# Performance work log

Measured on AMD Instinct MI355X. Metric: run time of the kernel, lower is better.

The kernel has to match this reference:

```python
import jax, jax.numpy as jnp
import numpy as np

H, C, PQ, PV = 12, 16, 4, 8   # heads, c_hidden, qk points, v points
CS, CZ = 384, 128
INF, EPS = 1e5, 1e-8


def quat_to_rot(q):
    w, x, y, z = q[..., 0], q[..., 1], q[..., 2], q[..., 3]
    r = jnp.stack([
        1 - 2 * (y * y + z * z), 2 * (x * y - w * z), 2 * (x * z + w * y),
        2 * (x * y + w * z), 1 - 2 * (x * x + z * z), 2 * (y * z - w * x),
        2 * (x * z - w * y), 2 * (y * z + w * x), 1 - 2 * (x * x + y * y)],
        axis=-1)
    return r.reshape(q.shape[:-1] + (3, 3))


def setup_inputs() -> dict:
    key = jax.random.key(0)
    ks = jax.random.split(key, 20)
    B, N = 1, 768
    s = jax.random.normal(ks[0], (B, N, CS), jnp.float32)
    z = jax.random.normal(ks[1], (B, N, N, CZ), jnp.float32)
    quat = jax.random.normal(ks[2], (B, N, 4), jnp.float32)
    quat = quat / jnp.linalg.norm(quat, axis=-1, keepdims=True)
    rot = quat_to_rot(quat)
    trans = 10.0 * jax.random.normal(ks[3], (B, N, 3), jnp.float32)
    mask = jnp.ones((B, N), jnp.float32)
    ss = jax.random.uniform(ks[4], (B, N, N), jnp.float32)
    sc = 0.02
    W_q = sc * jax.random.normal(ks[5], (CS, H * C), jnp.float32)
    b_q = jnp.zeros((H * C,), jnp.float32)
    W_kv = sc * jax.random.normal(ks[6], (CS, 2 * H * C), jnp.float32)
    b_kv = jnp.zeros((2 * H * C,), jnp.float32)
    W_qp = sc * jax.random.normal(ks[7], (CS, H * PQ * 3), jnp.float32)
    b_qp = jnp.zeros((H * PQ * 3,), jnp.float32)
    W_kvp = sc * jax.random.normal(ks[8], (CS, H * (PQ + PV) * 3), jnp.float32)
    b_kvp = jnp.zeros((H * (PQ + PV) * 3,), jnp.float32)
    W_b = sc * jax.random.normal(ks[9], (CZ, H), jnp.float32)
    b_b = jnp.zeros((H,), jnp.float32)
    head_weights = 0.1 * jax.random.normal(ks[10], (H,), jnp.float32)
    cdim = H * (CZ + C + PV * 4)
    W_out = sc * jax.random.normal(ks[11], (cdim, CS), jnp.float32)
    b_out = jnp.zeros((CS,), jnp.float32)
    return dict(s=s, z=z, rot=rot, trans=trans, mask=mask, ss=ss,
                W_q=W_q, b_q=b_q, W_kv=W_kv, b_kv=b_kv, W_qp=W_qp, b_qp=b_qp,
                W_kvp=W_kvp, b_kvp=b_kvp, W_b=W_b, b_b=b_b,
                head_weights=head_weights, W_out=W_out, b_out=b_out)


def reference(s, z, rot, trans, mask, ss, W_q, b_q, W_kv, b_kv, W_qp, b_qp,
              W_kvp, b_kvp, W_b, b_b, head_weights, W_out, b_out):
    B, N, _ = s.shape
    # scalar q/k/v  [B,N,H,C]
    q = (s @ W_q + b_q).reshape(B, N, H, C)
    kv = (s @ W_kv + b_kv).reshape(B, N, H, 2 * C)
    k, v = kv[..., :C], kv[..., C:]
    # point q/k/v: linear output is [x_all, y_all, z_all] -> stack on last dim
    qp = s @ W_qp + b_qp                                  # [B,N,H*PQ*3]
    qp = jnp.stack(jnp.split(qp, 3, axis=-1), axis=-1)    # [B,N,H*PQ,3] local
    qp = jnp.einsum('bnxy,bnpy->bnpx', rot, qp) + trans[:, :, None]
    qp = qp.reshape(B, N, H, PQ, 3)                       # global frame
    kvp = s @ W_kvp + b_kvp
    kvp = jnp.stack(jnp.split(kvp, 3, axis=-1), axis=-1)  # [B,N,H*(PQ+PV),3]
    kvp = jnp.einsum('bnxy,bnpy->bnpx', rot, kvp) + trans[:, :, None]
    kvp = kvp.reshape(B, N, H, PQ + PV, 3)
    kp, vp = kvp[..., :PQ, :], kvp[..., PQ:, :]
    # scalar attention logits + pair bias
    b = z @ W_b + b_b                                     # [B,N,N,H]
    a = jnp.einsum('bihc,bjhc->bhij', q, k) * np.sqrt(1.0 / (3 * C))
    a = a + np.sqrt(1.0 / 3) * jnp.transpose(b, (0, 3, 1, 2))
    # point-distance attention
    diff = qp[:, :, None] - kp[:, None]                   # [B,N,N,H,PQ,3]
    d2 = jnp.sum(diff * diff, axis=-1)                    # [B,N,N,H,PQ]
    hw = jax.nn.softplus(head_weights) * np.sqrt(1.0 / (3 * (PQ * 9.0 / 2)))
    pt = -0.5 * jnp.sum(d2 * hw[None, None, None, :, None], axis=-1)  # [B,N,N,H]
    a = a + jnp.transpose(pt, (0, 3, 1, 2))
    sq_mask = INF * (mask[:, :, None] * mask[:, None, :] - 1.0)
    a = a + sq_mask[:, None]
    # weighted softmax (ss_usage='multiply', t_ss=1): weights = exp(ss) - 0.99
    weights = jnp.exp(ss) - 0.99                          # [B,N,N]
    e = jnp.exp(a - jnp.max(a, axis=-1, keepdims=True))
    we = e * weights[:, None]
    a = we / jnp.sum(we, axis=-1, keepdims=True)          # [B,H,N,N]
    # outputs
    o = jnp.einsum('bhij,bjhc->bihc', a, v).reshape(B, N, H * C)
    o_pt = jnp.einsum('bhij,bjhpc->bihpc', a, vp)         # [B,N,H,PV,3] global
    o_pt = jnp.einsum('bnyx,bnhpy->bnhpx', rot, o_pt - trans[:, :, None, None])
    o_pt_norm = jnp.sqrt(jnp.sum(o_pt ** 2, axis=-1) + EPS).reshape(B, N, H * PV)
    o_pt = o_pt.reshape(B, N, H * PV, 3)
    o_pair = jnp.einsum('bhij,bijc->bihc', a, z).reshape(B, N, H * CZ)
    cat = jnp.concatenate(
        [o, o_pt[..., 0], o_pt[..., 1], o_pt[..., 2], o_pt_norm, o_pair], axis=-1)
    return cat @ W_out + b_out
```

## Files before the change

kernel.cpp:

```cpp
#include <hip/hip_runtime.h>
#include <math.h>

#define NN 768
#define CSD 384
#define HD 12
#define CD 16
#define PQD 4
#define PVD 8
#define CZD 128
#define CATD 2112

#define OFF_Q      0u
#define OFF_K      147456u
#define OFF_V      294912u
#define OFF_QP     442368u
#define OFF_KP     552960u
#define OFF_VP     663552u
#define OFF_RAW    884736u
#define OFF_B      1327104u
#define OFF_A      8404992u
#define OFF_CAT    15482880u

__device__ __forceinline__ float wcol_val(const float* Wq, const float* Wkv,
                                          const float* Wqp, const float* Wkvp,
                                          int k, int col) {
  if (col < 192) return Wq[k*192 + col];
  if (col < 576) return Wkv[k*384 + (col-192)];
  if (col < 720) return Wqp[k*144 + (col-576)];
  return Wkvp[k*432 + (col-720)];
}
__device__ __forceinline__ float bias_val(const float* bq, const float* bkv,
                                          const float* bqp, const float* bkvp, int col) {
  if (col < 192) return bq[col];
  if (col < 576) return bkv[col-192];
  if (col < 720) return bqp[col-576];
  return bkvp[col-720];
}

__global__ __launch_bounds__(256) void k_proj(const float* __restrict__ s,
    const float* __restrict__ Wq, const float* __restrict__ bq,
    const float* __restrict__ Wkv, const float* __restrict__ bkv,
    const float* __restrict__ Wqp, const float* __restrict__ bqp,
    const float* __restrict__ Wkvp, const float* __restrict__ bkvp,
    float* __restrict__ ws) {
  __shared__ float At[64*17];
  __shared__ float Bt[16*64];
  int t = threadIdx.x;
  int c0 = blockIdx.x * 64;
  int r0 = blockIdx.y * 64;
  float acc[4][4] = {};
  int cc = t & 15, rr = t >> 4;
  for (int kt = 0; kt < CSD; kt += 16) {
    int ka = t & 15, mb = t >> 4;
#pragma unroll
    for (int p = 0; p < 4; ++p) {
      int m = mb + p*16;
      At[m*17 + ka] = s[(r0+m)*CSD + kt + ka];
    }
    int cb = t & 63, kb = t >> 6;
#pragma unroll
    for (int p = 0; p < 4; ++p) {
      int kk = kb + p*4;
      Bt[kk*64 + cb] = wcol_val(Wq,Wkv,Wqp,Wkvp, kt+kk, c0+cb);
    }
    __syncthreads();
#pragma unroll
    for (int k = 0; k < 16; ++k) {
      float a0 = At[(rr*4+0)*17 + k];
      float a1 = At[(rr*4+1)*17 + k];
      float a2 = At[(rr*4+2)*17 + k];
      float a3 = At[(rr*4+3)*17 + k];
      float4 b4 = *(const float4*)&Bt[k*64 + cc*4];
      acc[0][0] = fmaf(a0,b4.x,acc[0][0]); acc[0][1] = fmaf(a0,b4.y,acc[0][1]);
      acc[0][2] = fmaf(a0,b4.z,acc[0][2]); acc[0][3] = fmaf(a0,b4.w,acc[0][3]);
      acc[1][0] = fmaf(a1,b4.x,acc[1][0]); acc[1][1] = fmaf(a1,b4.y,acc[1][1]);
      acc[1][2] = fmaf(a1,b4.z,acc[1][2]); acc[1][3] = fmaf(a1,b4.w,acc[1][3]);
      acc[2][0] = fmaf(a2,b4.x,acc[2][0]); acc[2][1] = fmaf(a2,b4.y,acc[2][1]);
      acc[2][2] = fmaf(a2,b4.z,acc[2][2]); acc[2][3] = fmaf(a2,b4.w,acc[2][3]);
      acc[3][0] = fmaf(a3,b4.x,acc[3][0]); acc[3][1] = fmaf(a3,b4.y,acc[3][1]);
      acc[3][2] = fmaf(a3,b4.z,acc[3][2]); acc[3][3] = fmaf(a3,b4.w,acc[3][3]);
    }
    __syncthreads();
  }
  float* qbuf = ws + OFF_Q; float* kbuf = ws + OFF_K; float* vbuf = ws + OFF_V;
  float* raw  = ws + OFF_RAW;
#pragma unroll
  for (int jj = 0; jj < 4; ++jj) {
    int col = c0 + cc*4 + jj;
    float bv = bias_val(bq,bkv,bqp,bkvp,col);
#pragma unroll
    for (int ii = 0; ii < 4; ++ii) {
      int row = r0 + rr*4 + ii;
      float val = acc[ii][jj] + bv;
      if (col < 192) {
        int h = col >> 4, c = col & 15;
        qbuf[(h*NN + row)*CD + c] = val;
      } else if (col < 576) {
        int u = col - 192; int h = u >> 5; int c2 = u & 31;
        if (c2 < 16) kbuf[(h*NN+row)*CD + c2] = val;
        else         vbuf[(h*NN+row)*CD + (c2-16)] = val;
      } else {
        raw[row*576 + (col-576)] = val;
      }
    }
  }
}

__global__ __launch_bounds__(256) void k_points(const float* __restrict__ rot,
    const float* __restrict__ trans, const float* __restrict__ bout,
    float* __restrict__ out, float* __restrict__ ws) {
  int bx = blockIdx.x;
  if (bx >= 576) {
    int idx = (bx - 576)*256 + threadIdx.x;
    out[idx] = bout[idx % CSD];
    return;
  }
  int tg = bx*256 + threadIdx.x;
  int n = tg / 192, pidx = tg % 192;
  const float* raw = ws + OFF_RAW + n*576;
  float v0, v1, v2;
  if (pidx < 48) { v0 = raw[pidx]; v1 = raw[48+pidx]; v2 = raw[96+pidx]; }
  else { int pp = pidx-48; v0 = raw[144+pp]; v1 = raw[288+pp]; v2 = raw[432+pp]; }
  const float* R = rot + n*9; const float* T = trans + n*3;
  float g0 = R[0]*v0 + R[1]*v1 + R[2]*v2 + T[0];
  float g1 = R[3]*v0 + R[4]*v1 + R[5]*v2 + T[1];
  float g2 = R[6]*v0 + R[7]*v1 + R[8]*v2 + T[2];
  if (pidx < 48) {
    int h = pidx >> 2, p = pidx & 3;
    float* qp = ws + OFF_QP + ((h*NN + n)*PQD + p)*3;
    qp[0]=g0; qp[1]=g1; qp[2]=g2;
  } else {
    int pp = pidx - 48; int h = pp/12; int q12 = pp - 12*h;
    if (q12 < 4) { float* kp = ws + OFF_KP + ((h*NN+n)*PQD + q12)*3; kp[0]=g0; kp[1]=g1; kp[2]=g2; }
    else         { float* vp = ws + OFF_VP + ((h*NN+n)*PVD + (q12-4))*3; vp[0]=g0; vp[1]=g1; vp[2]=g2; }
  }
}

#define BR 128
#define BPAD 130
__global__ __launch_bounds__(256) void k_bias(const float* __restrict__ z,
    const float* __restrict__ Wb, const float* __restrict__ bb, float* __restrict__ ws) {
  __shared__ float zt[BR*BPAD];
  int t = threadIdx.x;
  int q = t & 15;
  int rg = t >> 4;
  float wbr[8][12];
#pragma unroll
  for (int cc = 0; cc < 8; ++cc) {
    const float* wp = Wb + (q*8 + cc)*HD;
#pragma unroll
    for (int h = 0; h < 12; ++h) wbr[cc][h] = wp[h];
  }
  const int b3=(q>>3)&1, b2=(q>>2)&1, b1=(q>>1)&1, b0=q&1;
  const int hmine = 6*b3 + 3*b2 + (b1 ? 2 : b0);
  const bool writer = !(b1 && b0);
  const float bbh = bb[hmine];

  const int rowbase = blockIdx.x * 1152;
  float* bmat = ws + OFF_B;
  const float s2 = 0.57735026918962576f;

  for (int T = 0; T < 9; ++T) {
    int r0 = rowbase + T*BR;
#pragma unroll 4
    for (int it = 0; it < 16; ++it) {
      int g = it*256 + t;
      int row = g >> 5, f4 = g & 31;
      float4 v = *(const float4*)(z + (size_t)(r0+row)*CZD + f4*4);
      float* d = &zt[row*BPAD + f4*4];
      *(float2*)(d)   = make_float2(v.x, v.y);
      *(float2*)(d+2) = make_float2(v.z, v.w);
    }
    __syncthreads();
#pragma unroll 2
    for (int ps = 0; ps < 8; ++ps) {
      int row = ps*16 + rg;
      const float* zr = &zt[row*BPAD + q*8];
      float2 z01 = *(const float2*)(zr);
      float2 z23 = *(const float2*)(zr+2);
      float2 z45 = *(const float2*)(zr+4);
      float2 z67 = *(const float2*)(zr+6);
      float acc[12];
#pragma unroll
      for (int h = 0; h < 12; ++h) {
        float a = z01.x*wbr[0][h];
        a = fmaf(z01.y, wbr[1][h], a);
        a = fmaf(z23.x, wbr[2][h], a);
        a = fmaf(z23.y, wbr[3][h], a);
        a = fmaf(z45.x, wbr[4][h], a);
        a = fmaf(z45.y, wbr[5][h], a);
        a = fmaf(z67.x, wbr[6][h], a);
        a = fmaf(z67.y, wbr[7][h], a);
        acc[h] = a;
      }
      float na[6];
#pragma unroll
      for (int m = 0; m < 6; ++m) {
        float keep = b3 ? acc[m+6] : acc[m];
        float give = b3 ? acc[m]   : acc[m+6];
        na[m] = keep + __shfl_xor(give, 8);
      }
      float nb[3];
#pragma unroll
      for (int m = 0; m < 3; ++m) {
        float keep = b2 ? na[m+3] : na[m];
        float give = b2 ? na[m]   : na[m+3];
        nb[m] = keep + __shfl_xor(give, 4);
      }
      float k0 = b1 ? nb[2] : nb[0];
      float g0v = b1 ? nb[0] : nb[2];
      float k1 = b1 ? 0.f   : nb[1];
      float g1v = b1 ? nb[1] : 0.f;
      float c0v = k0 + __shfl_xor(g0v, 2);
      float c1v = k1 + __shfl_xor(g1v, 2);
      float k2 = b1 ? c0v : (b0 ? c1v : c0v);
      float g2v = b1 ? c0v : (b0 ? c0v : c1v);
      float d0 = k2 + __shfl_xor(g2v, 1);
      if (writer) {
        int r = r0 + row;
        int i = r / NN;
        int j = r - i*NN;
        bmat[((size_t)i*HD + hmine)*NN + j] = s2*(d0 + bbh);
      }
    }
    __syncthreads();
  }
}

__global__ __launch_bounds__(256) void k_fused(
    const float* __restrict__ z,
    const float* __restrict__ rot, const float* __restrict__ trans,
    const float* __restrict__ mask, const float* __restrict__ ss,
    const float* __restrict__ hwts, float* __restrict__ ws) {
  __shared__ float a_sm[HD*NN];
  __shared__ float4 psm[2][HD][32];
  __shared__ float wred[8];
  int i = blockIdx.x;
  int t = threadIdx.x;
  const float* qbuf = ws + OFF_Q; const float* kbuf = ws + OFF_K;
  const float* qp   = ws + OFF_QP; const float* kp  = ws + OFF_KP;
  const float* vbuf = ws + OFF_V;  const float* vpbuf = ws + OFF_VP;
  const float* bmat = ws + OFF_B;
  float* cat = ws + OFF_CAT;
  const float s1 = 0.14433756729740643f;

  float mi = mask[i];
  float msk3[3], ss3[3];
#pragma unroll
  for (int jj = 0; jj < 3; ++jj) {
    int j = t + jj*256;
    msk3[jj] = 100000.0f*(mi*mask[j] - 1.0f);
    ss3[jj]  = __expf(ss[i*NN + j]) - 0.99f;
  }

  for (int h = 0; h < HD; ++h) {
    const float4* qv4 = (const float4*)(qbuf + (h*NN+i)*CD);
    float4 q0 = qv4[0], q1 = qv4[1], q2 = qv4[2], q3 = qv4[3];
    const float4* qp4 = (const float4*)(qp + (h*NN+i)*12);
    float4 p0 = qp4[0], p1 = qp4[1], p2 = qp4[2];
    float coef = -0.5f * 0.13608276348795434f * log1pf(__expf(hwts[h]));
    float l3[3];
#pragma unroll
    for (int jj = 0; jj < 3; ++jj) {
      int j = t + jj*256;
      const float4* kb = (const float4*)(kbuf + (h*NN+j)*CD);
      float dot = 0.f;
      float4 kv;
      kv = kb[0];
      dot = fmaf(q0.x, kv.x, dot); dot = fmaf(q0.y, kv.y, dot);
      dot = fmaf(q0.z, kv.z, dot); dot = fmaf(q0.w, kv.w, dot);
      kv = kb[1];
      dot = fmaf(q1.x, kv.x, dot); dot = fmaf(q1.y, kv.y, dot);
      dot = fmaf(q1.z, kv.z, dot); dot = fmaf(q1.w, kv.w, dot);
      kv = kb[2];
      dot = fmaf(q2.x, kv.x, dot); dot = fmaf(q2.y, kv.y, dot);
      dot = fmaf(q2.z, kv.z, dot); dot = fmaf(q2.w, kv.w, dot);
      kv = kb[3];
      dot = fmaf(q3.x, kv.x, dot); dot = fmaf(q3.y, kv.y, dot);
      dot = fmaf(q3.z, kv.z, dot); dot = fmaf(q3.w, kv.w, dot);
      const float4* kpb = (const float4*)(kp + (h*NN+j)*12);
      float pts = 0.f; float d;
      float4 kpv;
      kpv = kpb[0];
      d = p0.x-kpv.x; pts = fmaf(d,d,pts);
      d = p0.y-kpv.y; pts = fmaf(d,d,pts);
      d = p0.z-kpv.z; pts = fmaf(d,d,pts);
      d = p0.w-kpv.w; pts = fmaf(d,d,pts);
      kpv = kpb[1];
      d = p1.x-kpv.x; pts = fmaf(d,d,pts);
      d = p1.y-kpv.y; pts = fmaf(d,d,pts);
      d = p1.z-kpv.z; pts = fmaf(d,d,pts);
      d = p1.w-kpv.w; pts = fmaf(d,d,pts);
      kpv = kpb[2];
      d = p2.x-kpv.x; pts = fmaf(d,d,pts);
      d = p2.y-kpv.y; pts = fmaf(d,d,pts);
      d = p2.z-kpv.z; pts = fmaf(d,d,pts);
      d = p2.w-kpv.w; pts = fmaf(d,d,pts);
      float bterm = bmat[((size_t)i*HD + h)*NN + j];
      l3[jj] = fmaf(dot, s1, bterm) + coef*pts + msk3[jj];
    }
    float mx = fmaxf(l3[0], fmaxf(l3[1], l3[2]));
#pragma unroll
    for (int off = 32; off >= 1; off >>= 1) mx = fmaxf(mx, __shfl_xor(mx, off));
    if ((t & 63) == 0) wred[t>>6] = mx;
    __syncthreads();
    mx = fmaxf(fmaxf(wred[0],wred[1]), fmaxf(wred[2],wred[3]));
    float e3[3]; float sum = 0.f;
#pragma unroll
    for (int jj = 0; jj < 3; ++jj) {
      e3[jj] = __expf(l3[jj]-mx) * ss3[jj];
      sum += e3[jj];
    }
#pragma unroll
    for (int off = 32; off >= 1; off >>= 1) sum += __shfl_xor(sum, off);
    if ((t & 63) == 0) wred[4 + (t>>6)] = sum;
    __syncthreads();
    sum = (wred[4]+wred[5]) + (wred[6]+wred[7]);
    float inv = 1.0f / sum;
#pragma unroll
    for (int jj = 0; jj < 3; ++jj)
      a_sm[h*NN + t + jj*256] = e3[jj]*inv;
  }
  __syncthreads();

  int wv = t >> 6, lane = t & 63;
  for (int hh = 0; hh < 3; ++hh) {
    int h = wv*3 + hh;
    float acc = 0.f;
    if (lane < 40) {
      const float* ptr; int stride;
      if (lane < 16) { ptr = vbuf + (size_t)(h*NN)*CD + lane; stride = CD; }
      else           { ptr = vpbuf + (size_t)(h*NN)*24 + (lane-16); stride = 24; }
      const float* arow = &a_sm[h*NN];
      for (int j = 0; j < NN; j += 4) {
        float4 a4 = *(const float4*)(arow + j);
        float x0 = ptr[0];
        float x1 = ptr[stride];
        float x2 = ptr[2*stride];
        float x3 = ptr[3*stride];
        ptr += 4*stride;
        acc = fmaf(a4.x, x0, acc);
        acc = fmaf(a4.y, x1, acc);
        acc = fmaf(a4.z, x2, acc);
        acc = fmaf(a4.w, x3, acc);
      }
    }
    if (lane < 16) {
      cat[(size_t)i*CATD + h*CD + lane] = acc;
    } else if (lane < 40) {
      int pv = lane - 16; int p = pv/3; int x = pv - 3*p;
      int base = 16 + p*3;
      float g0 = __shfl(acc, base+0);
      float g1 = __shfl(acc, base+1);
      float g2 = __shfl(acc, base+2);
      float v0 = g0 - trans[i*3+0];
      float v1 = g1 - trans[i*3+1];
      float v2 = g2 - trans[i*3+2];
      float loc = rot[i*9 + 0*3 + x]*v0 + rot[i*9 + 1*3 + x]*v1 + rot[i*9 + 2*3 + x]*v2;
      cat[(size_t)i*CATD + 192 + x*96 + h*PVD + p] = loc;
      float sq = loc*loc;
      float n2 = __shfl(sq, base+0) + __shfl(sq, base+1) + __shfl(sq, base+2);
      if (x == 0) cat[(size_t)i*CATD + 480 + h*PVD + p] = sqrtf(n2 + 1e-8f);
    }
  }

  int c4 = t & 31, jc = t >> 5;
  const float* zbase = z + ((size_t)i*NN + (size_t)jc*96)*CZD + c4*4;
  float4 acc[12];
#pragma unroll
  for (int h = 0; h < 12; ++h) acc[h] = make_float4(0.f,0.f,0.f,0.f);
  for (int jj = 0; jj < 96; jj += 4) {
    float4 z0 = *(const float4*)(zbase + (size_t)(jj+0)*CZD);
    float4 z1 = *(const float4*)(zbase + (size_t)(jj+1)*CZD);
    float4 z2 = *(const float4*)(zbase + (size_t)(jj+2)*CZD);
    float4 z3 = *(const float4*)(zbase + (size_t)(jj+3)*CZD);
    int j0 = jc*96 + jj;
#pragma unroll
    for (int h = 0; h < 12; ++h) {
      float4 av = *(const float4*)&a_sm[h*NN + j0];
      acc[h].x = fmaf(av.x, z0.x, acc[h].x); acc[h].y = fmaf(av.x, z0.y, acc[h].y);
      acc[h].z = fmaf(av.x, z0.z, acc[h].z); acc[h].w = fmaf(av.x, z0.w, acc[h].w);
      acc[h].x = fmaf(av.y, z1.x, acc[h].x); acc[h].y = fmaf(av.y, z1.y, acc[h].y);
      acc[h].z = fmaf(av.y, z1.z, acc[h].z); acc[h].w = fmaf(av.y, z1.w, acc[h].w);
      acc[h].x = fmaf(av.z, z2.x, acc[h].x); acc[h].y = fmaf(av.z, z2.y, acc[h].y);
      acc[h].z = fmaf(av.z, z2.z, acc[h].z); acc[h].w = fmaf(av.z, z2.w, acc[h].w);
      acc[h].x = fmaf(av.w, z3.x, acc[h].x); acc[h].y = fmaf(av.w, z3.y, acc[h].y);
      acc[h].z = fmaf(av.w, z3.z, acc[h].z); acc[h].w = fmaf(av.w, z3.w, acc[h].w);
    }
  }
  int ln = t & 63;
#pragma unroll
  for (int h = 0; h < 12; ++h) {
    acc[h].x += __shfl_down(acc[h].x, 32);
    acc[h].y += __shfl_down(acc[h].y, 32);
    acc[h].z += __shfl_down(acc[h].z, 32);
    acc[h].w += __shfl_down(acc[h].w, 32);
  }
  if (wv >= 2 && ln < 32) {
#pragma unroll
    for (int h = 0; h < 12; ++h) psm[wv-2][h][ln] = acc[h];
  }
  __syncthreads();
  if (wv < 2 && ln < 32) {
#pragma unroll
    for (int h = 0; h < 12; ++h) {
      float4 p = psm[wv][h][ln];
      acc[h].x += p.x; acc[h].y += p.y; acc[h].z += p.z; acc[h].w += p.w;
      psm[wv][h][ln] = acc[h];
    }
  }
  __syncthreads();
  for (int o = t; o < 384; o += 256) {
    int h = o >> 5, cc = o & 31;
    float4 s0 = psm[0][h][cc], s1 = psm[1][h][cc];
    float4 r;
    r.x = s0.x + s1.x;
    r.y = s0.y + s1.y;
    r.z = s0.z + s1.z;
    r.w = s0.w + s1.w;
    *(float4*)&cat[(size_t)i*CATD + 576 + h*CZD + cc*4] = r;
  }
}

__global__ __launch_bounds__(256) void k_final(const float* __restrict__ Wout,
    float* __restrict__ out, const float* __restrict__ ws) {
  __shared__ float At[64*17];
  __shared__ float Bt[16*64];
  const float* cat = ws + OFF_CAT;
  int t = threadIdx.x;
  int c0 = blockIdx.x*64, r0 = blockIdx.y*64;
  int kstart = blockIdx.z*528;
  float acc[4][4] = {};
  int cc = t & 15, rr = t >> 4;
  for (int kt = 0; kt < 528; kt += 16) {
    int ka = t & 15, mb = t >> 4;
#pragma unroll
    for (int p = 0; p < 4; ++p) {
      int m = mb + p*16;
      At[m*17 + ka] = cat[(size_t)(r0+m)*CATD + kstart + kt + ka];
    }
    int cb = t & 63, kb = t >> 6;
#pragma unroll
    for (int p = 0; p < 4; ++p) {
      int kk = kb + p*4;
      Bt[kk*64 + cb] = Wout[(size_t)(kstart+kt+kk)*CSD + c0 + cb];
    }
    __syncthreads();
#pragma unroll
    for (int k = 0; k < 16; ++k) {
      float a0 = At[(rr*4+0)*17 + k];
      float a1 = At[(rr*4+1)*17 + k];
      float a2 = At[(rr*4+2)*17 + k];
      float a3 = At[(rr*4+3)*17 + k];
      float4 b4 = *(const float4*)&Bt[k*64 + cc*4];
      acc[0][0] = fmaf(a0,b4.x,acc[0][0]); acc[0][1] = fmaf(a0,b4.y,acc[0][1]);
      acc[0][2] = fmaf(a0,b4.z,acc[0][2]); acc[0][3] = fmaf(a0,b4.w,acc[0][3]);
      acc[1][0] = fmaf(a1,b4.x,acc[1][0]); acc[1][1] = fmaf(a1,b4.y,acc[1][1]);
      acc[1][2] = fmaf(a1,b4.z,acc[1][2]); acc[1][3] = fmaf(a1,b4.w,acc[1][3]);
      acc[2][0] = fmaf(a2,b4.x,acc[2][0]); acc[2][1] = fmaf(a2,b4.y,acc[2][1]);
      acc[2][2] = fmaf(a2,b4.z,acc[2][2]); acc[2][3] = fmaf(a2,b4.w,acc[2][3]);
      acc[3][0] = fmaf(a3,b4.x,acc[3][0]); acc[3][1] = fmaf(a3,b4.y,acc[3][1]);
      acc[3][2] = fmaf(a3,b4.z,acc[3][2]); acc[3][3] = fmaf(a3,b4.w,acc[3][3]);
    }
    __syncthreads();
  }
#pragma unroll
  for (int ii = 0; ii < 4; ++ii)
#pragma unroll
    for (int jj = 0; jj < 4; ++jj)
      atomicAdd(&out[(size_t)(r0+rr*4+ii)*CSD + c0 + cc*4 + jj], acc[ii][jj]);
}

extern "C" void kernel_launch(void* const* d_in, const int* in_sizes, int n_in,
                              void* d_out, int out_size, void* d_ws, size_t ws_size,
                              hipStream_t stream) {
  const float* s    = (const float*)d_in[0];
  const float* z    = (const float*)d_in[1];
  const float* rot  = (const float*)d_in[2];
  const float* trans= (const float*)d_in[3];
  const float* mask = (const float*)d_in[4];
  const float* ss   = (const float*)d_in[5];
  const float* Wq   = (const float*)d_in[6];
  const float* bq   = (const float*)d_in[7];
  const float* Wkv  = (const float*)d_in[8];
  const float* bkv  = (const float*)d_in[9];
  const float* Wqp  = (const float*)d_in[10];
  const float* bqp  = (const float*)d_in[11];
  const float* Wkvp = (const float*)d_in[12];
  const float* bkvp = (const float*)d_in[13];
  const float* Wb   = (const float*)d_in[14];
  const float* bb   = (const float*)d_in[15];
  const float* hw   = (const float*)d_in[16];
  const float* Wout = (const float*)d_in[17];
  const float* bout = (const float*)d_in[18];
  float* ws  = (float*)d_ws;
  float* out = (float*)d_out;

  hipLaunchKernelGGL(k_proj, dim3(18,12), dim3(256), 0, stream,
                     s, Wq,bq, Wkv,bkv, Wqp,bqp, Wkvp,bkvp, ws);
  hipLaunchKernelGGL(k_points, dim3(1728), dim3(256), 0, stream, rot, trans, bout, out, ws);
  hipLaunchKernelGGL(k_bias, dim3(512), dim3(256), 0, stream, z, Wb, bb, ws);
  hipLaunchKernelGGL(k_fused, dim3(768), dim3(256), 0, stream, z, rot, trans, mask, ss, hw, ws);
  hipLaunchKernelGGL(k_final, dim3(6,12,4), dim3(256), 0, stream, Wout, out, ws);
}
```

Measured before the change: 737.7 us.

## Double-buffer z tiles in bias kernel and prefetch z rows in fused kernel

After: 735.6 us. About the same (-0.3%).

```diff
diff --git a/kernel.cpp b/kernel.cpp
--- a/kernel.cpp
+++ b/kernel.cpp
@@ -136,50 +136,63 @@
   }
 }
 
-#define BR 128
+#define BR2 48
 #define BPAD 130
 __global__ __launch_bounds__(256) void k_bias(const float* __restrict__ z,
     const float* __restrict__ Wb, const float* __restrict__ bb, float* __restrict__ ws) {
-  __shared__ float zt[BR*BPAD];
+  __shared__ float zt[2][BR2*BPAD];
   int t = threadIdx.x;
-  int q = t & 15;
-  int rg = t >> 4;
-  float wbr[8][12];
-#pragma unroll
-  for (int cc = 0; cc < 8; ++cc) {
-    const float* wp = Wb + (q*8 + cc)*HD;
+  int q = t & 31;
+  int rs = t >> 5;
+  float wbr[4][12];
+#pragma unroll
+  for (int cc = 0; cc < 4; ++cc) {
+    const float* wp = Wb + (q*4 + cc)*HD;
 #pragma unroll
     for (int h = 0; h < 12; ++h) wbr[cc][h] = wp[h];
   }
-  const int b3=(q>>3)&1, b2=(q>>2)&1, b1=(q>>1)&1, b0=q&1;
-  const int hmine = 6*b3 + 3*b2 + (b1 ? 2 : b0);
-  const bool writer = !(b1 && b0);
+  const int b4=(q>>4)&1, b3=(q>>3)&1, b2=(q>>2)&1, b1=(q>>1)&1, b0=q&1;
+  const int hmine = 6*b4 + 3*b3 + (b2 ? 2 : b1);
+  const bool writer = (b0 == 0) && (b2 == 0 || b1 == 0);
   const float bbh = bb[hmine];
 
-  const int rowbase = blockIdx.x * 1152;
-  float* bmat = ws + OFF_B;
+  const int i = blockIdx.x;
+  const float* zi = z + (size_t)i*NN*CZD;
+  float* bmat = ws + OFF_B + (size_t)i*HD*NN;
   const float s2 = 0.57735026918962576f;
 
-  for (int T = 0; T < 9; ++T) {
-    int r0 = rowbase + T*BR;
-#pragma unroll 4
-    for (int it = 0; it < 16; ++it) {
-      int g = it*256 + t;
-      int row = g >> 5, f4 = g & 31;
-      float4 v = *(const float4*)(z + (size_t)(r0+row)*CZD + f4*4);
-      float* d = &zt[row*BPAD + f4*4];
-      *(float2*)(d)   = make_float2(v.x, v.y);
-      *(float2*)(d+2) = make_float2(v.z, v.w);
-    }
-    __syncthreads();
-#pragma unroll 2
-    for (int ps = 0; ps < 8; ++ps) {
-      int row = ps*16 + rg;
-      const float* zr = &zt[row*BPAD + q*8];
+  float4 st[6];
+#pragma unroll
+  for (int it = 0; it < 6; ++it) {
+    int g = it*256 + t; int row = g >> 5, f4 = g & 31;
+    st[it] = *(const float4*)(zi + (size_t)row*CZD + f4*4);
+  }
+#pragma unroll
+  for (int it = 0; it < 6; ++it) {
+    int g = it*256 + t; int row = g >> 5, f4 = g & 31;
+    float* d = &zt[0][row*BPAD + f4*4];
+    *(float2*)(d)   = make_float2(st[it].x, st[it].y);
+    *(float2*)(d+2) = make_float2(st[it].z, st[it].w);
+  }
+  for (int T = 0; T < 16; ++T) {
+    const float* buf = zt[T & 1];
+    float* nbuf = zt[(T & 1) ^ 1];
+    __syncthreads();
+    if (T < 15) {
+      const float* zn = zi + (size_t)(T+1)*BR2*CZD;
+#pragma unroll
+      for (int it = 0; it < 6; ++it) {
+        int g = it*256 + t; int row = g >> 5, f4 = g & 31;
+        st[it] = *(const float4*)(zn + (size_t)row*CZD + f4*4);
+      }
+    }
+    int j0 = T*BR2;
+#pragma unroll
+    for (int ps = 0; ps < 6; ++ps) {
+      int row = ps*8 + rs;
+      const float* zr = &buf[row*BPAD + q*4];
       float2 z01 = *(const float2*)(zr);
       float2 z23 = *(const float2*)(zr+2);
-      float2 z45 = *(const float2*)(zr+4);
-      float2 z67 = *(const float2*)(zr+6);
       float acc[12];
 #pragma unroll
       for (int h = 0; h < 12; ++h) {
@@ -187,43 +200,46 @@
         a = fmaf(z01.y, wbr[1][h], a);
         a = fmaf(z23.x, wbr[2][h], a);
         a = fmaf(z23.y, wbr[3][h], a);
-        a = fmaf(z45.x, wbr[4][h], a);
-        a = fmaf(z45.y, wbr[5][h], a);
-        a = fmaf(z67.x, wbr[6][h], a);
-        a = fmaf(z67.y, wbr[7][h], a);
         acc[h] = a;
       }
       float na[6];
 #pragma unroll
       for (int m = 0; m < 6; ++m) {
-        float keep = b3 ? acc[m+6] : acc[m];
-        float give = b3 ? acc[m]   : acc[m+6];
-        na[m] = keep + __shfl_xor(give, 8);
+        float keep = b4 ? acc[m+6] : acc[m];
+        float give = b4 ? acc[m]   : acc[m+6];
+        na[m] = keep + __shfl_xor(give, 16);
       }
       float nb[3];
 #pragma unroll
       for (int m = 0; m < 3; ++m) {
-        float keep = b2 ? na[m+3] : na[m];
-        float give = b2 ? na[m]   : na[m+3];
-        nb[m] = keep + __shfl_xor(give, 4);
-      }
-      float k0 = b1 ? nb[2] : nb[0];
-      float g0v = b1 ? nb[0] : nb[2];
-      float k1 = b1 ? 0.f   : nb[1];
-      float g1v = b1 ? nb[1] : 0.f;
-      float c0v = k0 + __shfl_xor(g0v, 2);
-      float c1v = k1 + __shfl_xor(g1v, 2);
-      float k2 = b1 ? c0v : (b0 ? c1v : c0v);
-      float g2v = b1 ? c0v : (b0 ? c0v : c1v);
-      float d0 = k2 + __shfl_xor(g2v, 1);
+        float keep = b3 ? na[m+3] : na[m];
+        float give = b3 ? na[m]   : na[m+3];
+        nb[m] = keep + __shfl_xor(give, 8);
+      }
+      float k0 = b2 ? nb[2] : nb[0];
+      float g0v = b2 ? nb[0] : nb[2];
+      float k1 = b2 ? 0.f   : nb[1];
+      float g1v = b2 ? nb[1] : 0.f;
+      float c0v = k0 + __shfl_xor(g0v, 4);
+      float c1v = k1 + __shfl_xor(g1v, 4);
+      float k2 = b2 ? c0v : (b1 ? c1v : c0v);
+      float g2v = b2 ? c0v : (b1 ? c0v : c1v);
+      float d0 = k2 + __shfl_xor(g2v, 2);
+      float e0 = d0 + __shfl_xor(d0, 1);
       if (writer) {
-        int r = r0 + row;
-        int i = r / NN;
-        int j = r - i*NN;
-        bmat[((size_t)i*HD + hmine)*NN + j] = s2*(d0 + bbh);
-      }
-    }
-    __syncthreads();
+        int j = j0 + row;
+        bmat[(size_t)hmine*NN + j] = s2*(e0 + bbh);
+      }
+    }
+    if (T < 15) {
+#pragma unroll
+      for (int it = 0; it < 6; ++it) {
+        int g = it*256 + t; int row = g >> 5, f4 = g & 31;
+        float* d = &nbuf[row*BPAD + f4*4];
+        *(float2*)(d)   = make_float2(st[it].x, st[it].y);
+        *(float2*)(d+2) = make_float2(st[it].z, st[it].w);
+      }
+    }
   }
 }
 
@@ -369,11 +385,18 @@
   float4 acc[12];
 #pragma unroll
   for (int h = 0; h < 12; ++h) acc[h] = make_float4(0.f,0.f,0.f,0.f);
+  float4 zn0 = *(const float4*)(zbase);
+  float4 zn1 = *(const float4*)(zbase + (size_t)1*CZD);
+  float4 zn2 = *(const float4*)(zbase + (size_t)2*CZD);
+  float4 zn3 = *(const float4*)(zbase + (size_t)3*CZD);
   for (int jj = 0; jj < 96; jj += 4) {
-    float4 z0 = *(const float4*)(zbase + (size_t)(jj+0)*CZD);
-    float4 z1 = *(const float4*)(zbase + (size_t)(jj+1)*CZD);
-    float4 z2 = *(const float4*)(zbase + (size_t)(jj+2)*CZD);
-    float4 z3 = *(const float4*)(zbase + (size_t)(jj+3)*CZD);
+    float4 z0 = zn0, z1 = zn1, z2 = zn2, z3 = zn3;
+    if (jj < 92) {
+      zn0 = *(const float4*)(zbase + (size_t)(jj+4)*CZD);
+      zn1 = *(const float4*)(zbase + (size_t)(jj+5)*CZD);
+      zn2 = *(const float4*)(zbase + (size_t)(jj+6)*CZD);
+      zn3 = *(const float4*)(zbase + (size_t)(jj+7)*CZD);
+    }
     int j0 = jc*96 + jj;
 #pragma unroll
     for (int h = 0; h < 12; ++h) {
@@ -499,7 +522,7 @@
   hipLaunchKernelGGL(k_proj, dim3(18,12), dim3(256), 0, stream,
                      s, Wq,bq, Wkv,bkv, Wqp,bqp, Wkvp,bkvp, ws);
   hipLaunchKernelGGL(k_points, dim3(1728), dim3(256), 0, stream, rot, trans, bout, out, ws);
-  hipLaunchKernelGGL(k_bias, dim3(512), dim3(256), 0, stream, z, Wb, bb, ws);
+  hipLaunchKernelGGL(k_bias, dim3(768), dim3(256), 0, stream, z, Wb, bb, ws);
   hipLaunchKernelGGL(k_fused, dim3(768), dim3(256), 0, stream, z, rot, trans, mask, ss, hw, ws);
   hipLaunchKernelGGL(k_final, dim3(6,12,4), dim3(256), 0, stream, Wout, out, ws);
 }
```
